# Performance work log

Hardware: AMD Instinct MI355X
Metric: run time of the kernel (lower is better)

## Reference

```python
import jax, jax.numpy as jnp
import numpy as np

I = 6156  # input feature size
O = 3     # output classes
B = 2048  # batch


def setup_inputs() -> dict:
    key = jax.random.key(0)
    ks = jax.random.split(key, 6)
    x = jax.random.normal(ks[0], (B, I), dtype=jnp.float32)
    # nn.Linear(input_size, output_size)
    lin_w = jax.random.normal(ks[1], (O, I), dtype=jnp.float32) * (1.0 / np.sqrt(I))
    lin_b = jax.random.normal(ks[2], (O,), dtype=jnp.float32) * 0.01
    # interaction_weights: xavier_uniform_ on (I, I)
    limit = float(np.sqrt(6.0 / (I + I)))
    w_int = jax.random.uniform(ks[3], (I, I), dtype=jnp.float32, minval=-limit, maxval=limit)
    # final_layer: nn.Linear(I + O, O)
    fin_w = jax.random.normal(ks[4], (O, I + O), dtype=jnp.float32) * (1.0 / np.sqrt(I + O))
    fin_b = jax.random.normal(ks[5], (O,), dtype=jnp.float32) * 0.01
    return {"x": x, "lin_w": lin_w, "lin_b": lin_b, "w_int": w_int,
            "fin_w": fin_w, "fin_b": fin_b}


def reference(x, lin_w, lin_b, w_int, fin_w, fin_b):
    # linear_logits = x @ lin_w.T + lin_b  -> [B, O]
    linear_logits = x @ lin_w.T + lin_b
    # einsum('bi,bj,ij->bij').sum(dim=2) == x * (x @ w_int.T)
    # GEMM [B,I]x[I,I] + elementwise multiply; no O(B*I*I) intermediate.
    interactions = x * (x @ w_int.T)  # [B, I]
    combined = jnp.concatenate([linear_logits, interactions], axis=1)  # [B, O+I]
    logits = combined @ fin_w.T + fin_b  # [B, O]
    return logits
```

## Files before the change

kernel.cpp:

```cpp
#include <hip/hip_runtime.h>
#include <hip/hip_bf16.h>

constexpr int Bsz = 2048;
constexpr int Iin = 6156;
constexpr int IF  = 6159;
constexpr int Kp  = 6208;
constexpr int NpW = 6400;
constexpr int MT  = Bsz / 256;
constexpr int NTN = 25;

typedef __attribute__((ext_vector_type(8))) short short8;
typedef __attribute__((ext_vector_type(4))) float f32x4;
typedef __attribute__((ext_vector_type(4))) int   i32x4;

#define AS1 __attribute__((address_space(1)))
#define AS3 __attribute__((address_space(3)))

__device__ __forceinline__ short f2bf(float f) {
    union { float f; unsigned u; } v; v.f = f;
    unsigned r = v.u + 0x7FFFu + ((v.u >> 16) & 1u);
    return (short)(r >> 16);
}

__device__ __forceinline__ short8 pack8(float4 a, float4 b) {
    short8 r;
    r[0] = f2bf(a.x); r[1] = f2bf(a.y); r[2] = f2bf(a.z); r[3] = f2bf(a.w);
    r[4] = f2bf(b.x); r[5] = f2bf(b.y); r[6] = f2bf(b.z); r[7] = f2bf(b.w);
    return r;
}

__device__ __forceinline__ void stage_chunk(const void* src, const void* ldsbase) {
    __builtin_amdgcn_global_load_lds((const AS1 void*)src, (AS3 void*)ldsbase, 16, 0, 0);
}

__global__ __launch_bounds__(256) void quant_x_linear_kernel(
    const float* __restrict__ x, const float* __restrict__ lin_w,
    const float* __restrict__ lin_b, const float* __restrict__ fin_w,
    const float* __restrict__ fin_b,
    signed char* __restrict__ dst, float* __restrict__ scales,
    float* __restrict__ out) {
    __shared__ float rowbuf[Kp];
    __shared__ float redm[4], red0[4], red1[4], red2[4];
    int row = blockIdx.x;
    int t   = threadIdx.x;
    const float4* s  = (const float4*)(x + (size_t)row * Iin);
    const float4* w0 = (const float4*)(lin_w);
    const float4* w1 = (const float4*)(lin_w + Iin);
    const float4* w2 = (const float4*)(lin_w + 2 * Iin);
    float amax = 0.f, s0 = 0.f, s1 = 0.f, s2 = 0.f;
    for (int i = t; i < Iin / 4; i += 256) {
        float4 v = s[i];
        ((float4*)rowbuf)[i] = v;
        amax = fmaxf(amax, fmaxf(fmaxf(fabsf(v.x), fabsf(v.y)),
                                 fmaxf(fabsf(v.z), fabsf(v.w))));
        float4 a0 = w0[i], a1 = w1[i], a2 = w2[i];
        s0 += v.x * a0.x + v.y * a0.y + v.z * a0.z + v.w * a0.w;
        s1 += v.x * a1.x + v.y * a1.y + v.z * a1.z + v.w * a1.w;
        s2 += v.x * a2.x + v.y * a2.y + v.z * a2.z + v.w * a2.w;
    }
    for (int i = Iin + t; i < Kp; i += 256) rowbuf[i] = 0.f;
    #pragma unroll
    for (int off = 1; off < 64; off <<= 1) {
        amax = fmaxf(amax, __shfl_xor(amax, off, 64));
        s0 += __shfl_xor(s0, off, 64);
        s1 += __shfl_xor(s1, off, 64);
        s2 += __shfl_xor(s2, off, 64);
    }
    if ((t & 63) == 0) {
        int w = t >> 6;
        redm[w] = amax; red0[w] = s0; red1[w] = s1; red2[w] = s2;
    }
    __syncthreads();
    float am = fmaxf(fmaxf(redm[0], redm[1]), fmaxf(redm[2], redm[3]));
    float rs = (am > 0.f) ? 127.f / am : 0.f;
    if (t == 0) {
        scales[row] = (am > 0.f) ? am / 127.f : 0.f;
        float l0 = red0[0] + red0[1] + red0[2] + red0[3] + lin_b[0];
        float l1 = red1[0] + red1[1] + red1[2] + red1[3] + lin_b[1];
        float l2 = red2[0] + red2[1] + red2[2] + red2[3] + lin_b[2];
        #pragma unroll
        for (int o = 0; o < 3; ++o) {
            out[row * 3 + o] = fin_b[o]
                + fin_w[(size_t)o * IF + 0] * l0
                + fin_w[(size_t)o * IF + 1] * l1
                + fin_w[(size_t)o * IF + 2] * l2;
        }
    }
    int xorv = (row >> 1) & 3;
    for (int p = t; p < Kp / 16; p += 256) {
        int blk = p >> 2, sub = p & 3;
        int sc  = (blk << 6) + ((sub ^ xorv) << 4);
        i32x4 pk;
        #pragma unroll
        for (int j = 0; j < 4; ++j) {
            unsigned u = 0;
            #pragma unroll
            for (int e = 0; e < 4; ++e) {
                float v = rowbuf[sc + j * 4 + e] * rs;
                int q = (int)rintf(v);
                q = q > 127 ? 127 : (q < -127 ? -127 : q);
                u |= ((unsigned)(q & 255)) << (8 * e);
            }
            pk[j] = (int)u;
        }
        *(i32x4*)(dst + (size_t)row * Kp + (size_t)p * 16) = pk;
    }
}

__global__ __launch_bounds__(256) void quant_kernel(
    const float* __restrict__ src, signed char* __restrict__ dst,
    float* __restrict__ scales, int src_rows) {
    __shared__ float rowbuf[Kp];
    __shared__ float red[4];
    int row = blockIdx.x;
    int t   = threadIdx.x;
    float amax = 0.f;
    if (row < src_rows) {
        const float4* s = (const float4*)(src + (size_t)row * Iin);
        for (int i = t; i < Iin / 4; i += 256) {
            float4 v = s[i];
            ((float4*)rowbuf)[i] = v;
            amax = fmaxf(amax, fmaxf(fmaxf(fabsf(v.x), fabsf(v.y)),
                                     fmaxf(fabsf(v.z), fabsf(v.w))));
        }
        for (int i = Iin + t; i < Kp; i += 256) rowbuf[i] = 0.f;
    } else {
        for (int i = t; i < Kp; i += 256) rowbuf[i] = 0.f;
    }
    #pragma unroll
    for (int off = 1; off < 64; off <<= 1)
        amax = fmaxf(amax, __shfl_xor(amax, off, 64));
    if ((t & 63) == 0) red[t >> 6] = amax;
    __syncthreads();
    float am = fmaxf(fmaxf(red[0], red[1]), fmaxf(red[2], red[3]));
    float rs = (am > 0.f) ? 127.f / am : 0.f;
    if (t == 0) scales[row] = (am > 0.f) ? am / 127.f : 0.f;

    int xorv = (row >> 1) & 3;
    for (int p = t; p < Kp / 16; p += 256) {
        int blk = p >> 2, sub = p & 3;
        int sc  = (blk << 6) + ((sub ^ xorv) << 4);
        i32x4 pk;
        #pragma unroll
        for (int j = 0; j < 4; ++j) {
            unsigned u = 0;
            #pragma unroll
            for (int e = 0; e < 4; ++e) {
                float v = rowbuf[sc + j * 4 + e] * rs;
                int q = (int)rintf(v);
                q = q > 127 ? 127 : (q < -127 ? -127 : q);
                u |= ((unsigned)(q & 255)) << (8 * e);
            }
            pk[j] = (int)u;
        }
        *(i32x4*)(dst + (size_t)row * Kp + (size_t)p * 16) = pk;
    }
}

__global__ __launch_bounds__(512, 2) void gemm_i8(
    const signed char* __restrict__ xq, const signed char* __restrict__ wq,
    const float* __restrict__ sx, const float* __restrict__ sw,
    const float* __restrict__ xf, const float* __restrict__ finw,
    float* __restrict__ out) {

    __shared__ signed char lsA[4][16384];
    __shared__ signed char lsB[4][16384];
    __shared__ float part[256][3];

    const int tid  = threadIdx.x;
    const int lane = tid & 63;
    const int wid  = tid >> 6;
    const int wr   = wid >> 2;
    const int wc   = wid & 3;
    const int l15  = lane & 15;
    const int koff = (((lane >> 4) ^ ((lane >> 1) & 3)) << 4);

    int swz = ((int)blockIdx.x & 7) * NTN + ((int)blockIdx.x >> 3);
    int tm = swz & 7;
    int tn = swz >> 3;
    int bm0 = tm << 8;
    int in0 = tn << 8;

    i32x4 acc[8][4];
    #pragma unroll
    for (int m = 0; m < 8; ++m)
        #pragma unroll
        for (int n = 0; n < 4; ++n)
            acc[m][n] = (i32x4){0, 0, 0, 0};

    auto stageA = [&](int tk, int h, int slot) {
        int idx = h * 512 + tid;
        int row = idx >> 2, sub = idx & 3;
        const signed char* src = xq + (size_t)(bm0 + row) * Kp + tk * 64 + sub * 16;
        stage_chunk(src, &lsA[slot][(size_t)idx * 16]);
    };
    auto stageB = [&](int tk, int h, int slot) {
        int idx = h * 512 + tid;
        int row = idx >> 2, sub = idx & 3;
        const signed char* src = wq + (size_t)(in0 + row) * Kp + tk * 64 + sub * 16;
        stage_chunk(src, &lsB[slot][(size_t)idx * 16]);
    };
    auto ldA = [&](int slot, int m) -> i32x4 {
        int row = wr * 128 + m * 16 + l15;
        return *(const i32x4*)&lsA[slot][row * 64 + koff];
    };
    auto ldB = [&](int slot, int n) -> i32x4 {
        int row = wc * 64 + n * 16 + l15;
        return *(const i32x4*)&lsB[slot][row * 64 + koff];
    };

    i32x4 afA[8], afB[8], bf[4];

    stageA(0, 0, 0); stageA(0, 1, 0); stageB(0, 0, 0); stageB(0, 1, 0);
    stageA(1, 0, 1); stageA(1, 1, 1); stageB(1, 0, 1); stageB(1, 1, 1);
    stageA(2, 0, 2); stageA(2, 1, 2); stageB(2, 0, 2); stageB(2, 1, 2);
    asm volatile("s_waitcnt vmcnt(8)" ::: "memory");
    __builtin_amdgcn_s_barrier();
    #pragma unroll
    for (int m = 0; m < 8; ++m) afA[m] = ldA(0, m);

#define SEC(T, SL, NSL, SSL, CUR, NXT, TW, DO_PF, DO_ST)                  \
    {                                                                     \
        asm volatile("s_waitcnt " TW ::: "memory");                       \
        __builtin_amdgcn_s_barrier();                                     \
        _Pragma("unroll")                                                 \
        for (int n = 0; n < 4; ++n) bf[n] = ldB(SL, n);                   \
        __builtin_amdgcn_sched_barrier(0);                                \
        if (DO_PF) {                                                      \
            _Pragma("unroll")                                             \
            for (int m = 0; m < 8; ++m) NXT[m] = ldA(NSL, m);             \
        }                                                                 \
        __builtin_amdgcn_sched_barrier(0);                                \
        if (DO_ST) {                                                      \
            stageA((T) + 3, 0, SSL); stageA((T) + 3, 1, SSL);             \
            stageB((T) + 3, 0, SSL); stageB((T) + 3, 1, SSL);             \
        }                                                                 \
        __builtin_amdgcn_sched_barrier(0);                                \
        if (DO_PF) { asm volatile("s_waitcnt lgkmcnt(8)" ::: "memory"); } \
        else       { asm volatile("s_waitcnt lgkmcnt(0)" ::: "memory"); } \
        __builtin_amdgcn_sched_barrier(0);                                \
        __builtin_amdgcn_s_setprio(1);                                    \
        _Pragma("unroll")                                                 \
        for (int m = 0; m < 8; ++m)                                       \
            _Pragma("unroll")                                             \
            for (int n = 0; n < 4; ++n)                                   \
                acc[m][n] = __builtin_amdgcn_mfma_i32_16x16x64_i8(        \
                    CUR[m], bf[n], acc[m][n], 0, 0, 0);                   \
        __builtin_amdgcn_s_setprio(0);                                    \
        __builtin_amdgcn_sched_barrier(0);                                \
    }

    for (int i = 0; i < 23; ++i) {
        int t = 4 * i;
        SEC(t,     0, 1, 3, afA, afB, "vmcnt(4)", true, true);
        SEC(t + 1, 1, 2, 0, afB, afA, "vmcnt(4)", true, true);
        SEC(t + 2, 2, 3, 1, afA, afB, "vmcnt(4)", true, true);
        SEC(t + 3, 3, 0, 2, afB, afA, "vmcnt(4)", true, true);
    }
    SEC(92, 0, 1, 3, afA, afB, "vmcnt(4)", true, true);
    SEC(93, 1, 2, 0, afB, afA, "vmcnt(4)", true, true);
    SEC(94, 2, 3, 1, afA, afB, "vmcnt(4)", true, false);
    SEC(95, 3, 0, 2, afB, afA, "vmcnt(0)", true, false);
    SEC(96, 0, 1, 3, afA, afB, "vmcnt(0)", false, false);
#undef SEC

    __syncthreads();
    for (int t = tid; t < 768; t += 512) ((float*)part)[t] = 0.f;
    __syncthreads();

    int q4 = lane >> 4;
    #pragma unroll
    for (int m = 0; m < 8; ++m) {
        #pragma unroll
        for (int r = 0; r < 4; ++r) {
            int lr = wr * 128 + m * 16 + q4 * 4 + r;
            int bg = bm0 + lr;
            float sxv = sx[bg];
            float s0 = 0.f, s1 = 0.f, s2 = 0.f;
            #pragma unroll
            for (int n = 0; n < 4; ++n) {
                int gi = in0 + wc * 64 + n * 16 + l15;
                if (gi < Iin) {
                    float z = (float)acc[m][n][r] * sxv * sw[gi];
                    float inter = z * xf[(size_t)bg * Iin + gi];
                    s0 += inter * finw[(size_t)0 * IF + 3 + gi];
                    s1 += inter * finw[(size_t)1 * IF + 3 + gi];
                    s2 += inter * finw[(size_t)2 * IF + 3 + gi];
                }
            }
            #pragma unroll
            for (int off = 1; off < 16; off <<= 1) {
                s0 += __shfl_xor(s0, off, 64);
                s1 += __shfl_xor(s1, off, 64);
                s2 += __shfl_xor(s2, off, 64);
            }
            if (l15 == 0) {
                atomicAdd(&part[lr][0], s0);
                atomicAdd(&part[lr][1], s1);
                atomicAdd(&part[lr][2], s2);
            }
        }
    }
    __syncthreads();
    for (int t = tid; t < 768; t += 512) {
        int lr = t / 3, o = t - lr * 3;
        atomicAdd(&out[(size_t)(bm0 + lr) * 3 + o], part[lr][o]);
    }
}

__global__ void linear_init_kernel(const float* __restrict__ x,
                                   const float* __restrict__ lin_w,
                                   const float* __restrict__ lin_b,
                                   const float* __restrict__ fin_w,
                                   const float* __restrict__ fin_b,
                                   float* __restrict__ out) {
    int wid  = threadIdx.x >> 6;
    int lane = threadIdx.x & 63;
    int b = blockIdx.x * 4 + wid;
    if (b >= Bsz) return;
    const float4* xr = (const float4*)(x + (size_t)b * Iin);
    const float4* w0 = (const float4*)(lin_w);
    const float4* w1 = (const float4*)(lin_w + Iin);
    const float4* w2 = (const float4*)(lin_w + 2 * Iin);
    float s0 = 0.f, s1 = 0.f, s2 = 0.f;
    for (int i = lane; i < Iin / 4; i += 64) {
        float4 xv = xr[i];
        float4 a0 = w0[i], a1 = w1[i], a2 = w2[i];
        s0 += xv.x * a0.x + xv.y * a0.y + xv.z * a0.z + xv.w * a0.w;
        s1 += xv.x * a1.x + xv.y * a1.y + xv.z * a1.z + xv.w * a1.w;
        s2 += xv.x * a2.x + xv.y * a2.y + xv.z * a2.z + xv.w * a2.w;
    }
    #pragma unroll
    for (int off = 1; off < 64; off <<= 1) {
        s0 += __shfl_xor(s0, off, 64);
        s1 += __shfl_xor(s1, off, 64);
        s2 += __shfl_xor(s2, off, 64);
    }
    if (lane == 0) {
        float l0 = s0 + lin_b[0], l1 = s1 + lin_b[1], l2 = s2 + lin_b[2];
        #pragma unroll
        for (int o = 0; o < 3; ++o) {
            out[b * 3 + o] = fin_b[o]
                + fin_w[(size_t)o * IF + 0] * l0
                + fin_w[(size_t)o * IF + 1] * l1
                + fin_w[(size_t)o * IF + 2] * l2;
        }
    }
}

__global__ __launch_bounds__(256) void gemm_fallback(
    const float* __restrict__ xf, const float* __restrict__ wf,
    const float* __restrict__ finw, float* __restrict__ out) {

    __shared__ short lsA[128 * 64];
    __shared__ short lsB[128 * 64];
    __shared__ float part[128][3];

    int tid  = threadIdx.x;
    int lane = tid & 63;
    int wid  = tid >> 6;
    int wm   = wid & 1;
    int wn   = wid >> 1;

    int ntiles = (Bsz / 128) * (6272 / 128);
    int tile = (blockIdx.x & 7) * (ntiles >> 3) + (blockIdx.x >> 3);
    int tm = tile & 15;
    int tn = tile >> 4;
    int bm0 = tm << 7;
    int in0 = tn << 7;

    f32x4 acc[4][4];
    #pragma unroll
    for (int m = 0; m < 4; ++m)
        #pragma unroll
        for (int n = 0; n < 4; ++n)
            acc[m][n] = (f32x4){0.f, 0.f, 0.f, 0.f};

    for (int k0 = 0; k0 < Kp; k0 += 64) {
        #pragma unroll
        for (int it = 0; it < 4; ++it) {
            int idx = it * 256 + tid;
            int r   = idx >> 3;
            int seg = idx & 7;
            int kc  = k0 + seg * 8;
            int sd  = (seg ^ (r & 7)) << 3;
            {
                const float* s = xf + (size_t)(bm0 + r) * Iin + kc;
                short8 st;
                if (kc + 8 <= Iin) {
                    float4 f0 = *(const float4*)s;
                    float4 f1 = *(const float4*)(s + 4);
                    st = pack8(f0, f1);
                } else {
                    #pragma unroll
                    for (int e = 0; e < 8; ++e) {
                        float v = (kc + e < Iin) ? s[e] : 0.f;
                        st[e] = f2bf(v);
                    }
                }
                *(short8*)&lsA[r * 64 + sd] = st;
            }
            {
                int grow = in0 + r;
                short8 st;
                if (grow < Iin && kc + 8 <= Iin) {
                    const float* s = wf + (size_t)grow * Iin + kc;
                    float4 f0 = *(const float4*)s;
                    float4 f1 = *(const float4*)(s + 4);
                    st = pack8(f0, f1);
                } else if (grow < Iin) {
                    const float* s = wf + (size_t)grow * Iin + kc;
                    #pragma unroll
                    for (int e = 0; e < 8; ++e) {
                        float v = (kc + e < Iin) ? s[e] : 0.f;
                        st[e] = f2bf(v);
                    }
                } else {
                    #pragma unroll
                    for (int e = 0; e < 8; ++e) st[e] = 0;
                }
                *(short8*)&lsB[r * 64 + sd] = st;
            }
        }
        __syncthreads();

        #pragma unroll
        for (int kk = 0; kk < 2; ++kk) {
            int q = (kk << 2) + (lane >> 4);
            short8 af[4], bfr[4];
            #pragma unroll
            for (int m = 0; m < 4; ++m) {
                int R = wm * 64 + m * 16 + (lane & 15);
                af[m] = *(const short8*)&lsA[R * 64 + ((q ^ (R & 7)) << 3)];
            }
            #pragma unroll
            for (int n = 0; n < 4; ++n) {
                int R = wn * 64 + n * 16 + (lane & 15);
                bfr[n] = *(const short8*)&lsB[R * 64 + ((q ^ (R & 7)) << 3)];
            }
            #pragma unroll
            for (int m = 0; m < 4; ++m)
                #pragma unroll
                for (int n = 0; n < 4; ++n)
                    acc[m][n] = __builtin_amdgcn_mfma_f32_16x16x32_bf16(
                        af[m], bfr[n], acc[m][n], 0, 0, 0);
        }
        __syncthreads();
    }

    for (int t = tid; t < 384; t += 256) ((float*)part)[t] = 0.f;
    __syncthreads();

    #pragma unroll
    for (int m = 0; m < 4; ++m) {
        int rowbase = bm0 + wm * 64 + m * 16 + ((lane >> 4) << 2);
        #pragma unroll
        for (int r = 0; r < 4; ++r) {
            int b = rowbase + r;
            float s0 = 0.f, s1 = 0.f, s2 = 0.f;
            #pragma unroll
            for (int n = 0; n < 4; ++n) {
                int gi = in0 + wn * 64 + n * 16 + (lane & 15);
                if (gi < Iin) {
                    float inter = acc[m][n][r] * xf[(size_t)b * Iin + gi];
                    s0 += inter * finw[(size_t)0 * IF + 3 + gi];
                    s1 += inter * finw[(size_t)1 * IF + 3 + gi];
                    s2 += inter * finw[(size_t)2 * IF + 3 + gi];
                }
            }
            #pragma unroll
            for (int off = 1; off < 16; off <<= 1) {
                s0 += __shfl_xor(s0, off, 64);
                s1 += __shfl_xor(s1, off, 64);
                s2 += __shfl_xor(s2, off, 64);
            }
            if ((lane & 15) == 0) {
                int lr = b - bm0;
                atomicAdd(&part[lr][0], s0);
                atomicAdd(&part[lr][1], s1);
                atomicAdd(&part[lr][2], s2);
            }
        }
    }
    __syncthreads();
    for (int t = tid; t < 384; t += 256) {
        int lr = t / 3, o = t - lr * 3;
        atomicAdd(&out[(size_t)(bm0 + lr) * 3 + o], part[lr][o]);
    }
}

extern "C" void kernel_launch(void* const* d_in, const int* in_sizes, int n_in,
                              void* d_out, int out_size, void* d_ws, size_t ws_size,
                              hipStream_t stream) {
    const float* x     = (const float*)d_in[0];
    const float* lin_w = (const float*)d_in[1];
    const float* lin_b = (const float*)d_in[2];
    const float* w_int = (const float*)d_in[3];
    const float* fin_w = (const float*)d_in[4];
    const float* fin_b = (const float*)d_in[5];
    float* out = (float*)d_out;

    const size_t xq_bytes = (size_t)Bsz * Kp;
    const size_t wq_bytes = (size_t)NpW * Kp;
    const size_t sx_off   = xq_bytes + wq_bytes;
    const size_t need = sx_off + (Bsz + NpW) * sizeof(float);

    if (ws_size >= need) {
        signed char* xq = (signed char*)d_ws;
        signed char* wq = xq + xq_bytes;
        float* sxp = (float*)((char*)d_ws + sx_off);
        float* swp = sxp + Bsz;
        quant_x_linear_kernel<<<Bsz, 256, 0, stream>>>(
            x, lin_w, lin_b, fin_w, fin_b, xq, sxp, out);
        quant_kernel<<<NpW, 256, 0, stream>>>(w_int, wq, swp, Iin);
        gemm_i8<<<MT * NTN, 512, 0, stream>>>(xq, wq, sxp, swp, x, fin_w, out);
    } else {
        linear_init_kernel<<<Bsz / 4, 256, 0, stream>>>(x, lin_w, lin_b, fin_w, fin_b, out);
        const int ntiles = (Bsz / 128) * (6272 / 128);
        gemm_fallback<<<ntiles, 256, 0, stream>>>(x, w_int, fin_w, out);
    }
}
```

Before: 165.9 us.

## Restructure int8 GEMM to double-buffered 128-wide K tiles with 8-way swizzle

Replaces the 4-slot, 64-byte-K LDS ring (three tiles in flight) with two slots of 128-byte K tiles, so each barrier covers two MFMA sub-steps and there are half as many barrier/wait rounds. Padded K grows to a multiple of 128 and the quantization swizzle widens to 8 groups of 16 bytes to match the new LDS row layout. The price is a shallower prefetch: every section waits for vmcnt(0), so global-load latency is hidden by only one tile of compute, and the padding adds zero work. The fp32 fallback loop is pinned to the old K bound.

```diff
diff --git a/kernel.cpp b/kernel.cpp
--- a/kernel.cpp
+++ b/kernel.cpp
@@ -4,8 +4,9 @@
 constexpr int Bsz = 2048;
 constexpr int Iin = 6156;
 constexpr int IF  = 6159;
-constexpr int Kp  = 6208;
+constexpr int Kp  = 6272;
 constexpr int NpW = 6400;
+constexpr int NSEC = Kp / 128;
 constexpr int MT  = Bsz / 256;
 constexpr int NTN = 25;
 
@@ -86,10 +87,10 @@
                 + fin_w[(size_t)o * IF + 2] * l2;
         }
     }
-    int xorv = (row >> 1) & 3;
+    int xorv = (row >> 1) & 7;
     for (int p = t; p < Kp / 16; p += 256) {
-        int blk = p >> 2, sub = p & 3;
-        int sc  = (blk << 6) + ((sub ^ xorv) << 4);
+        int blk = p >> 3, sub = p & 7;
+        int sc  = (blk << 7) + ((sub ^ xorv) << 4);
         i32x4 pk;
         #pragma unroll
         for (int j = 0; j < 4; ++j) {
@@ -136,10 +137,10 @@
     float rs = (am > 0.f) ? 127.f / am : 0.f;
     if (t == 0) scales[row] = (am > 0.f) ? am / 127.f : 0.f;
 
-    int xorv = (row >> 1) & 3;
+    int xorv = (row >> 1) & 7;
     for (int p = t; p < Kp / 16; p += 256) {
-        int blk = p >> 2, sub = p & 3;
-        int sc  = (blk << 6) + ((sub ^ xorv) << 4);
+        int blk = p >> 3, sub = p & 7;
+        int sc  = (blk << 7) + ((sub ^ xorv) << 4);
         i32x4 pk;
         #pragma unroll
         for (int j = 0; j < 4; ++j) {
@@ -163,8 +164,8 @@
     const float* __restrict__ xf, const float* __restrict__ finw,
     float* __restrict__ out) {
 
-    __shared__ signed char lsA[4][16384];
-    __shared__ signed char lsB[4][16384];
+    __shared__ signed char lsA[2][32768];
+    __shared__ signed char lsB[2][32768];
     __shared__ float part[256][3];
 
     const int tid  = threadIdx.x;
@@ -173,7 +174,8 @@
     const int wr   = wid >> 2;
     const int wc   = wid & 3;
     const int l15  = lane & 15;
-    const int koff = (((lane >> 4) ^ ((lane >> 1) & 3)) << 4);
+    const int rxor = l15 >> 1;
+    const int ghi  = lane >> 4;
 
     int swz = ((int)blockIdx.x & 7) * NTN + ((int)blockIdx.x >> 3);
     int tm = swz & 7;
@@ -188,56 +190,57 @@
         for (int n = 0; n < 4; ++n)
             acc[m][n] = (i32x4){0, 0, 0, 0};
 
-    auto stageA = [&](int tk, int h, int slot) {
-        int idx = h * 512 + tid;
-        int row = idx >> 2, sub = idx & 3;
-        const signed char* src = xq + (size_t)(bm0 + row) * Kp + tk * 64 + sub * 16;
-        stage_chunk(src, &lsA[slot][(size_t)idx * 16]);
+    auto stageA = [&](int tk, int slot) {
+        #pragma unroll
+        for (int it = 0; it < 4; ++it) {
+            int idx = it * 512 + tid;
+            int row = idx >> 3, g = idx & 7;
+            const signed char* src = xq + (size_t)(bm0 + row) * Kp + tk * 128 + g * 16;
+            stage_chunk(src, &lsA[slot][(size_t)idx * 16]);
+        }
     };
-    auto stageB = [&](int tk, int h, int slot) {
-        int idx = h * 512 + tid;
-        int row = idx >> 2, sub = idx & 3;
-        const signed char* src = wq + (size_t)(in0 + row) * Kp + tk * 64 + sub * 16;
-        stage_chunk(src, &lsB[slot][(size_t)idx * 16]);
+    auto stageB = [&](int tk, int slot) {
+        #pragma unroll
+        for (int it = 0; it < 4; ++it) {
+            int idx = it * 512 + tid;
+            int row = idx >> 3, g = idx & 7;
+            const signed char* src = wq + (size_t)(in0 + row) * Kp + tk * 128 + g * 16;
+            stage_chunk(src, &lsB[slot][(size_t)idx * 16]);
+        }
     };
-    auto ldA = [&](int slot, int m) -> i32x4 {
-        int row = wr * 128 + m * 16 + l15;
-        return *(const i32x4*)&lsA[slot][row * 64 + koff];
+    auto ldA = [&](int slot, int par, int m) -> i32x4 {
+        int row  = wr * 128 + m * 16 + l15;
+        int koff = (((par << 2) | ghi) ^ rxor) << 4;
+        return *(const i32x4*)&lsA[slot][row * 128 + koff];
     };
-    auto ldB = [&](int slot, int n) -> i32x4 {
-        int row = wc * 64 + n * 16 + l15;
-        return *(const i32x4*)&lsB[slot][row * 64 + koff];
+    auto ldB = [&](int slot, int par, int n) -> i32x4 {
+        int row  = wc * 64 + n * 16 + l15;
+        int koff = (((par << 2) | ghi) ^ rxor) << 4;
+        return *(const i32x4*)&lsB[slot][row * 128 + koff];
     };
 
-    i32x4 afA[8], afB[8], bf[4];
-
-    stageA(0, 0, 0); stageA(0, 1, 0); stageB(0, 0, 0); stageB(0, 1, 0);
-    stageA(1, 0, 1); stageA(1, 1, 1); stageB(1, 0, 1); stageB(1, 1, 1);
-    stageA(2, 0, 2); stageA(2, 1, 2); stageB(2, 0, 2); stageB(2, 1, 2);
-    asm volatile("s_waitcnt vmcnt(8)" ::: "memory");
-    __builtin_amdgcn_s_barrier();
-    #pragma unroll
-    for (int m = 0; m < 8; ++m) afA[m] = ldA(0, m);
-
-#define SEC(T, SL, NSL, SSL, CUR, NXT, TW, DO_PF, DO_ST)                  \
+    i32x4 af0[8], af1[8], bf[4];
+
+    stageA(0, 0); stageB(0, 0);
+
+#define SEC(T, SL, DO_ST)                                                 \
     {                                                                     \
-        asm volatile("s_waitcnt " TW ::: "memory");                       \
+        asm volatile("s_waitcnt vmcnt(0)" ::: "memory");                  \
         __builtin_amdgcn_s_barrier();                                     \
         _Pragma("unroll")                                                 \
-        for (int n = 0; n < 4; ++n) bf[n] = ldB(SL, n);                   \
-        __builtin_amdgcn_sched_barrier(0);                                \
-        if (DO_PF) {                                                      \
-            _Pragma("unroll")                                             \
-            for (int m = 0; m < 8; ++m) NXT[m] = ldA(NSL, m);             \
-        }                                                                 \
-        __builtin_amdgcn_sched_barrier(0);                                \
-        if (DO_ST) {                                                      \
-            stageA((T) + 3, 0, SSL); stageA((T) + 3, 1, SSL);             \
-            stageB((T) + 3, 0, SSL); stageB((T) + 3, 1, SSL);             \
-        }                                                                 \
-        __builtin_amdgcn_sched_barrier(0);                                \
-        if (DO_PF) { asm volatile("s_waitcnt lgkmcnt(8)" ::: "memory"); } \
-        else       { asm volatile("s_waitcnt lgkmcnt(0)" ::: "memory"); } \
+        for (int m = 0; m < 8; ++m) af0[m] = ldA(SL, 0, m);               \
+        __builtin_amdgcn_sched_barrier(0);                                \
+        if (DO_ST) stageA((T) + 1, (SL) ^ 1);                             \
+        __builtin_amdgcn_sched_barrier(0);                                \
+        _Pragma("unroll")                                                 \
+        for (int n = 0; n < 4; ++n) bf[n] = ldB(SL, 0, n);                \
+        __builtin_amdgcn_sched_barrier(0);                                \
+        if (DO_ST) stageB((T) + 1, (SL) ^ 1);                             \
+        __builtin_amdgcn_sched_barrier(0);                                \
+        _Pragma("unroll")                                                 \
+        for (int m = 0; m < 8; ++m) af1[m] = ldA(SL, 1, m);               \
+        __builtin_amdgcn_sched_barrier(0);                                \
+        asm volatile("s_waitcnt lgkmcnt(8)" ::: "memory");                \
         __builtin_amdgcn_sched_barrier(0);                                \
         __builtin_amdgcn_s_setprio(1);                                    \
         _Pragma("unroll")                                                 \
@@ -245,23 +248,30 @@
             _Pragma("unroll")                                             \
             for (int n = 0; n < 4; ++n)                                   \
                 acc[m][n] = __builtin_amdgcn_mfma_i32_16x16x64_i8(        \
-                    CUR[m], bf[n], acc[m][n], 0, 0, 0);                   \
+                    af0[m], bf[n], acc[m][n], 0, 0, 0);                   \
         __builtin_amdgcn_s_setprio(0);                                    \
         __builtin_amdgcn_sched_barrier(0);                                \
-    }
-
-    for (int i = 0; i < 23; ++i) {
-        int t = 4 * i;
-        SEC(t,     0, 1, 3, afA, afB, "vmcnt(4)", true, true);
-        SEC(t + 1, 1, 2, 0, afB, afA, "vmcnt(4)", true, true);
-        SEC(t + 2, 2, 3, 1, afA, afB, "vmcnt(4)", true, true);
-        SEC(t + 3, 3, 0, 2, afB, afA, "vmcnt(4)", true, true);
-    }
-    SEC(92, 0, 1, 3, afA, afB, "vmcnt(4)", true, true);
-    SEC(93, 1, 2, 0, afB, afA, "vmcnt(4)", true, true);
-    SEC(94, 2, 3, 1, afA, afB, "vmcnt(4)", true, false);
-    SEC(95, 3, 0, 2, afB, afA, "vmcnt(0)", true, false);
-    SEC(96, 0, 1, 3, afA, afB, "vmcnt(0)", false, false);
+        _Pragma("unroll")                                                 \
+        for (int n = 0; n < 4; ++n) bf[n] = ldB(SL, 1, n);                \
+        __builtin_amdgcn_sched_barrier(0);                                \
+        asm volatile("s_waitcnt lgkmcnt(0)" ::: "memory");                \
+        __builtin_amdgcn_sched_barrier(0);                                \
+        __builtin_amdgcn_s_setprio(1);                                    \
+        _Pragma("unroll")                                                 \
+        for (int m = 0; m < 8; ++m)                                       \
+            _Pragma("unroll")                                             \
+            for (int n = 0; n < 4; ++n)                                   \
+                acc[m][n] = __builtin_amdgcn_mfma_i32_16x16x64_i8(        \
+                    af1[m], bf[n], acc[m][n], 0, 0, 0);                   \
+        __builtin_amdgcn_s_setprio(0);                                    \
+        __builtin_amdgcn_sched_barrier(0);                                \
+    }
+
+    for (int i = 0; i < 24; ++i) {
+        SEC(2 * i,     0, true);
+        SEC(2 * i + 1, 1, true);
+    }
+    SEC(48, 0, false);
 #undef SEC
 
     __syncthreads();
@@ -376,7 +386,7 @@
         for (int n = 0; n < 4; ++n)
             acc[m][n] = (f32x4){0.f, 0.f, 0.f, 0.f};
 
-    for (int k0 = 0; k0 < Kp; k0 += 64) {
+    for (int k0 = 0; k0 < 6208; k0 += 64) {
         #pragma unroll
         for (int it = 0; it < 4; ++it) {
             int idx = it * 256 + tid;
```

Measured after the change: 186.3 us. 12.3% more time.
